# Kernel tuning notes

Measured on AMD Instinct MI355X. Metric: run time of the kernel, lower is better.

The kernel has to match this reference:

```python
import jax, jax.numpy as jnp
from jax import lax
import numpy as np

S, N, E = 4, 50000, 800000
D_IN, D_NOISE, D_H, D_OUT = 96, 32, 32, 128
F_CAT = D_IN + D_NOISE + D_H  # 160, matches nn.Linear(input_dim+noise_dim+32, out)


def setup_inputs() -> dict:
    key = jax.random.key(0)
    ks = jax.random.split(key, 8)
    X = jax.random.normal(ks[0], (1, N, D_IN), dtype=jnp.float32)
    h = jax.random.normal(ks[1], (1, N, D_H), dtype=jnp.float32)
    # Bernoulli(0.5) noise, sampled in setup for determinism (original samples in forward)
    epsilon = (jax.random.uniform(ks[2], (S, N, D_NOISE)) < 0.5).astype(jnp.float32)
    W = jax.random.normal(ks[3], (F_CAT, D_OUT), dtype=jnp.float32) * 0.02
    b = jnp.zeros((D_OUT,), dtype=jnp.float32)
    gin_eps = jnp.zeros((), dtype=jnp.float32)  # init_eps=0, learn_eps=True
    src = jax.random.randint(ks[4], (E,), 0, N, dtype=jnp.int32)
    dst = jax.random.randint(ks[5], (E,), 0, N, dtype=jnp.int32)
    return {"X": X, "h": h, "epsilon": epsilon, "W": W, "b": b,
            "gin_eps": gin_eps, "src": src, "dst": dst}


def reference(X, h, epsilon, W, b, gin_eps, src, dst):
    # X: [1,N,D_IN] expanded to sample_size; h: [1,N,32] expanded; epsilon: [S,N,D_NOISE]
    s, n = epsilon.shape[0], X.shape[1]
    Xb = jnp.broadcast_to(X, (s, n, X.shape[2]))
    hb = jnp.broadcast_to(h, (s, n, h.shape[2]))
    x_all = jnp.concatenate([Xb, epsilon, hb], axis=2)  # [S,N,F_CAT]

    def per_sample(carry, x):  # x: [N,F_CAT]
        # GINConv('sum'): (1+eps)*x + sum_{j in N(i)} x_j, then Linear, then activation
        agg = (1.0 + gin_eps) * x + jax.ops.segment_sum(x[src], dst, num_segments=n)
        y = jax.nn.relu(agg @ W + b)           # [N,D_OUT]
        return carry, jnp.mean(y, axis=0)      # per-layer mean over nodes -> [D_OUT]

    _, means = lax.scan(per_sample, None, x_all)  # [S,D_OUT]
    # outputTensor[i] = tempdim12 broadcasts the [D_OUT] vector over the node axis
    out = jnp.broadcast_to(means[:, None, :], (s, n, W.shape[1]))
    return jax.nn.relu(out), epsilon
```

## Files before the change

kernel.cpp:

```cpp
#include <hip/hip_runtime.h>

#define N_NODES  50000
#define N_EDGES  800000
#define D_OUTF   128
#define F_PACK   256
#define NTILES   3125
#define GEMM_BLOCKS 512
#define NB1      196
#define PBX 6250
#define PBB 25000
#define PBZ 196
#define PB_TOT (PBX + PBB + PBZ + 1)

typedef __attribute__((ext_vector_type(8))) short bf16x8;
typedef __attribute__((ext_vector_type(4))) float f32x4;
typedef __attribute__((ext_vector_type(2))) float f32x2;

__device__ __forceinline__ unsigned short f2bf(float x) {
  unsigned int u = __float_as_uint(x);
  u += 0x7FFFu + ((u >> 16) & 1u);
  return (unsigned short)(u >> 16);
}
__device__ __forceinline__ float bflo(unsigned int u) { return __uint_as_float(u << 16); }
__device__ __forceinline__ float bfhi(unsigned int u) { return __uint_as_float(u & 0xFFFF0000u); }
__device__ __forceinline__ unsigned int pack2(float a, float b) {
  return (unsigned int)f2bf(a) | ((unsigned int)f2bf(b) << 16);
}
__device__ __forceinline__ unsigned int spreadLo(unsigned int rep) {
  return (((rep & 0x08040201u) + 0x7F7F7F7Fu) >> 7) & 0x01010101u;
}
__device__ __forceinline__ unsigned int spreadHi(unsigned int rep) {
  return (((rep & 0x80402010u) + 0x7F7F7F7Fu) >> 7) & 0x01010101u;
}
__device__ __forceinline__ void f8acc(unsigned int w, float& a0, float& a1,
                                      float& a2, float& a3) {
  f32x2 p0 = __builtin_amdgcn_cvt_pk_f32_fp8(w, false);
  f32x2 p1 = __builtin_amdgcn_cvt_pk_f32_fp8(w, true);
  a0 += p0.x; a1 += p0.y; a2 += p1.x; a3 += p1.y;
}

__global__ void k_pack(const float* __restrict__ X, const float* __restrict__ h,
                       const float* __restrict__ eps,
                       unsigned int* __restrict__ featF8,
                       unsigned int* __restrict__ epsb, int* __restrict__ cnt,
                       float* __restrict__ sums) {
  int blk = blockIdx.x, tid = threadIdx.x;
  if (blk < PBX) {
    int t = blk * 256 + tid;
    int node = t >> 5, f = (t & 31) << 2;
    float a0, a1, a2, a3;
    if (f < 96) {
      const float* p = X + node * 96 + f;
      a0 = p[0]; a1 = p[1]; a2 = p[2]; a3 = p[3];
    } else {
      const float* p = h + node * 32 + (f - 96);
      a0 = p[0]; a1 = p[1]; a2 = p[2]; a3 = p[3];
    }
    unsigned int d = __builtin_amdgcn_cvt_pk_fp8_f32(a0, a1, 0, false);
    d = __builtin_amdgcn_cvt_pk_fp8_f32(a2, a3, d, true);
    featF8[t] = d;
  } else if (blk < PBX + PBB) {
    long g = (long)(blk - PBX) * 256 + tid;
    float v = eps[g];
    unsigned long long m = __ballot(v > 0.5f);
    int lane = tid & 63;
    if ((lane & 31) == 0) {
      long idx = g >> 5;
      int s = (int)(idx / N_NODES);
      int node = (int)(idx - (long)s * N_NODES);
      epsb[node * 4 + s] = (unsigned int)(m >> ((lane >> 5) * 32));
    }
  } else if (blk < PBX + PBB + PBZ) {
    int i = (blk - PBX - PBB) * 256 + tid;
    if (i < N_NODES) cnt[i] = 0;
  } else {
    sums[tid] = 0.f;
    sums[tid + 256] = 0.f;
  }
}

__global__ void k_hist(const int* __restrict__ dst, int* __restrict__ cnt) {
  int i = blockIdx.x * blockDim.x + threadIdx.x;
  if (i < N_EDGES) atomicAdd(&cnt[dst[i]], 1);
}

__global__ void k_scan1(const int* __restrict__ cnt, int* __restrict__ excl,
                        int* __restrict__ bsum) {
  __shared__ int wpart[4];
  int tid = threadIdx.x, lane = tid & 63, wid = tid >> 6;
  int i = blockIdx.x * 256 + tid;
  int v = (i < N_NODES) ? cnt[i] : 0;
  int x = v;
#pragma unroll
  for (int d = 1; d < 64; d <<= 1) {
    int t = __shfl_up(x, d, 64);
    if (lane >= d) x += t;
  }
  if (lane == 63) wpart[wid] = x;
  __syncthreads();
  if (tid == 0) {
    int s = 0;
#pragma unroll
    for (int w = 0; w < 4; ++w) { int t = wpart[w]; wpart[w] = s; s += t; }
    bsum[blockIdx.x] = s;
  }
  __syncthreads();
  if (i < N_NODES) excl[i] = wpart[wid] + x - v;
}

__global__ void k_scan2(const int* __restrict__ bsum, int* __restrict__ boff) {
  __shared__ int sd[256];
  int tid = threadIdx.x;
  int v = (tid < NB1) ? bsum[tid] : 0;
  sd[tid] = v;
  __syncthreads();
  for (int d = 1; d < 256; d <<= 1) {
    int t = (tid >= d) ? sd[tid - d] : 0;
    __syncthreads();
    sd[tid] += t;
    __syncthreads();
  }
  if (tid < NB1) boff[tid] = sd[tid] - v;
}

__global__ void k_scatter(const int* __restrict__ src, const int* __restrict__ dst,
                          const int* __restrict__ excl, const int* __restrict__ boff,
                          int* __restrict__ cnt, int* __restrict__ csr) {
  int i = blockIdx.x * blockDim.x + threadIdx.x;
  if (i < N_EDGES) {
    int d = dst[i];
    int r = atomicAdd(&cnt[d], -1);
    csr[excl[d] + boff[d >> 8] + r - 1] = src[i];
  }
}

__global__ __launch_bounds__(256) void k_agg_ep(
    const uint2* __restrict__ feat2, const unsigned int* __restrict__ epsw,
    const float* __restrict__ geps_p, const int* __restrict__ excl,
    const int* __restrict__ boff, const int* __restrict__ csr,
    uint4* __restrict__ agg4) {
  int wave = (blockIdx.x * blockDim.x + threadIdx.x) >> 6;
  int lane = threadIdx.x & 63;
  int li = lane & 15, es = lane >> 4;
  if (wave >= N_NODES) return;
  int n = wave;
  float ge = 1.0f + geps_p[0];
  int wsel = li >> 2, bsh = (li & 3) * 8;

  int off_n = excl[n] + boff[n >> 8];
  int e1 = (n == N_NODES - 1) ? N_EDGES : excl[n + 1] + boff[(n + 1) >> 8];

  uint2 sf = feat2[n * 16 + li];
  unsigned int swd = epsw[n * 4 + wsel];

  float af0 = 0.f, af1 = 0.f, af2 = 0.f, af3 = 0.f;
  float af4 = 0.f, af5 = 0.f, af6 = 0.f, af7 = 0.f;
  unsigned int accLo = 0, accHi = 0;

  int e = off_n + es;
  for (; e + 4 < e1; e += 8) {
    int s0 = csr[e], s1 = csr[e + 4];
    uint2 f0 = feat2[s0 * 16 + li];
    uint2 f1 = feat2[s1 * 16 + li];
    unsigned int w0 = epsw[s0 * 4 + wsel];
    unsigned int w1 = epsw[s1 * 4 + wsel];
    f8acc(f0.x, af0, af1, af2, af3);  f8acc(f0.y, af4, af5, af6, af7);
    f8acc(f1.x, af0, af1, af2, af3);  f8acc(f1.y, af4, af5, af6, af7);
    unsigned int B0 = (w0 >> bsh) & 0xFFu;
    unsigned int B1 = (w1 >> bsh) & 0xFFu;
    unsigned int r0 = B0 | (B0 << 8);  r0 |= r0 << 16;
    unsigned int r1 = B1 | (B1 << 8);  r1 |= r1 << 16;
    accLo += spreadLo(r0) + spreadLo(r1);
    accHi += spreadHi(r0) + spreadHi(r1);
  }
  if (e < e1) {
    int s0 = csr[e];
    uint2 f0 = feat2[s0 * 16 + li];
    unsigned int w0 = epsw[s0 * 4 + wsel];
    f8acc(f0.x, af0, af1, af2, af3);  f8acc(f0.y, af4, af5, af6, af7);
    unsigned int B0 = (w0 >> bsh) & 0xFFu;
    unsigned int r0 = B0 | (B0 << 8);  r0 |= r0 << 16;
    accLo += spreadLo(r0);
    accHi += spreadHi(r0);
  }

#pragma unroll
  for (int d = 16; d < 64; d <<= 1) {
    af0 += __shfl_xor(af0, d, 64);  af1 += __shfl_xor(af1, d, 64);
    af2 += __shfl_xor(af2, d, 64);  af3 += __shfl_xor(af3, d, 64);
    af4 += __shfl_xor(af4, d, 64);  af5 += __shfl_xor(af5, d, 64);
    af6 += __shfl_xor(af6, d, 64);  af7 += __shfl_xor(af7, d, 64);
    accLo += __shfl_xor((int)accLo, d, 64);
    accHi += __shfl_xor((int)accHi, d, 64);
  }

  if (es == 0) {
    f32x2 s0 = __builtin_amdgcn_cvt_pk_f32_fp8(sf.x, false);
    f32x2 s1 = __builtin_amdgcn_cvt_pk_f32_fp8(sf.x, true);
    f32x2 s2 = __builtin_amdgcn_cvt_pk_f32_fp8(sf.y, false);
    f32x2 s3 = __builtin_amdgcn_cvt_pk_f32_fp8(sf.y, true);
    af0 += ge * s0.x;  af1 += ge * s0.y;
    af2 += ge * s1.x;  af3 += ge * s1.y;
    af4 += ge * s2.x;  af5 += ge * s2.y;
    af6 += ge * s3.x;  af7 += ge * s3.y;
    unsigned int Bself = (swd >> bsh) & 0xFFu;
    float ev0 = ge * (float)(Bself & 1u)        + (float)(accLo & 0xFFu);
    float ev1 = ge * (float)((Bself >> 1) & 1u) + (float)((accLo >> 8) & 0xFFu);
    float ev2 = ge * (float)((Bself >> 2) & 1u) + (float)((accLo >> 16) & 0xFFu);
    float ev3 = ge * (float)((Bself >> 3) & 1u) + (float)((accLo >> 24) & 0xFFu);
    float ev4 = ge * (float)((Bself >> 4) & 1u) + (float)(accHi & 0xFFu);
    float ev5 = ge * (float)((Bself >> 5) & 1u) + (float)((accHi >> 8) & 0xFFu);
    float ev6 = ge * (float)((Bself >> 6) & 1u) + (float)((accHi >> 16) & 0xFFu);
    float ev7 = ge * (float)((Bself >> 7) & 1u) + (float)((accHi >> 24) & 0xFFu);

    uint4 oXh, oEp;
    oXh.x = pack2(af0, af1); oXh.y = pack2(af2, af3);
    oXh.z = pack2(af4, af5); oXh.w = pack2(af6, af7);
    oEp.x = pack2(ev0, ev1); oEp.y = pack2(ev2, ev3);
    oEp.z = pack2(ev4, ev5); oEp.w = pack2(ev6, ev7);
    agg4[n * 32 + li]      = oXh;
    agg4[n * 32 + 16 + li] = oEp;
  }
}

__global__ __launch_bounds__(256) void k_gemm(const unsigned short* __restrict__ agg,
    const float* __restrict__ W, const float* __restrict__ b,
    float* __restrict__ sums) {
  int tid = threadIdx.x;
  int lane = tid & 63;
  int w = tid >> 6;
  int col = lane & 15;
  int quad = lane >> 4;

  bf16x8 Bsh[2][4];
  bf16x8 Bep[2];
  float bias[2];
#pragma unroll
  for (int i = 0; i < 2; ++i) {
    int obase = (2 * w + i) * 16;
    bias[i] = b[obase + col];
#pragma unroll
    for (int kb = 0; kb < 4; ++kb) {
      bf16x8 f;
#pragma unroll
      for (int j = 0; j < 8; ++j) {
        int k = kb * 32 + quad * 8 + j;
        int wr = (k < 96) ? k : k + 32;
        f[j] = (short)f2bf(W[wr * D_OUTF + obase + col]);
      }
      Bsh[i][kb] = f;
    }
    bf16x8 g;
#pragma unroll
    for (int j = 0; j < 8; ++j)
      g[j] = (short)f2bf(W[(96 + quad * 8 + j) * D_OUTF + obase + col]);
    Bep[i] = g;
  }

  f32x4 psum[4][2];
#pragma unroll
  for (int s = 0; s < 4; ++s)
#pragma unroll
    for (int i = 0; i < 2; ++i) psum[s][i] = (f32x4){0.f, 0.f, 0.f, 0.f};

  for (int t = blockIdx.x; t < NTILES; t += gridDim.x) {
    const unsigned short* arow = agg + (long)(t * 16 + col) * F_PACK;
    bf16x8 Ash[4];
#pragma unroll
    for (int kb = 0; kb < 4; ++kb)
      Ash[kb] = *(const bf16x8*)(arow + kb * 32 + quad * 8);
    f32x4 csh[2];
    csh[0] = (f32x4){0.f, 0.f, 0.f, 0.f};
    csh[1] = (f32x4){0.f, 0.f, 0.f, 0.f};
#pragma unroll
    for (int kb = 0; kb < 4; ++kb) {
      csh[0] = __builtin_amdgcn_mfma_f32_16x16x32_bf16(Ash[kb], Bsh[0][kb], csh[0], 0, 0, 0);
      csh[1] = __builtin_amdgcn_mfma_f32_16x16x32_bf16(Ash[kb], Bsh[1][kb], csh[1], 0, 0, 0);
    }
#pragma unroll
    for (int s = 0; s < 4; ++s) {
      bf16x8 Aep = *(const bf16x8*)(arow + 128 + s * 32 + quad * 8);
#pragma unroll
      for (int i = 0; i < 2; ++i) {
        f32x4 c = __builtin_amdgcn_mfma_f32_16x16x32_bf16(Aep, Bep[i], csh[i], 0, 0, 0);
#pragma unroll
        for (int r = 0; r < 4; ++r)
          psum[s][i][r] += fmaxf(c[r] + bias[i], 0.f);
      }
    }
  }

#pragma unroll
  for (int s = 0; s < 4; ++s)
#pragma unroll
    for (int i = 0; i < 2; ++i) {
      float v = psum[s][i][0] + psum[s][i][1] + psum[s][i][2] + psum[s][i][3];
      v += __shfl_xor(v, 16, 64);
      v += __shfl_xor(v, 32, 64);
      if (quad == 0)
        atomicAdd(&sums[s * 128 + (2 * w + i) * 16 + col], v);
    }
}

#define OUT0_F4 6400000L
#define EPS_F4  1600000L
#define INV_N   (1.0f / (float)N_NODES)
__global__ void k_out(const float* __restrict__ sums, const float* __restrict__ eps,
                      float* __restrict__ out) {
  long i = (long)blockIdx.x * blockDim.x + threadIdx.x;
  if (i < OUT0_F4) {
    int o4 = (int)(i & 31);
    long sn = i >> 5;
    int s = (int)(sn / N_NODES);
    float4 sv = ((const float4*)sums)[s * 32 + o4];
    float4 ov;
    ov.x = fmaxf(sv.x * INV_N, 0.f);
    ov.y = fmaxf(sv.y * INV_N, 0.f);
    ov.z = fmaxf(sv.z * INV_N, 0.f);
    ov.w = fmaxf(sv.w * INV_N, 0.f);
    ((float4*)out)[i] = ov;
  } else if (i < OUT0_F4 + EPS_F4) {
    long j = i - OUT0_F4;
    ((float4*)out)[OUT0_F4 + j] = ((const float4*)eps)[j];
  }
}

extern "C" void kernel_launch(void* const* d_in, const int* in_sizes, int n_in,
                              void* d_out, int out_size, void* d_ws, size_t ws_size,
                              hipStream_t stream) {
  const float* X    = (const float*)d_in[0];
  const float* h    = (const float*)d_in[1];
  const float* eps  = (const float*)d_in[2];
  const float* W    = (const float*)d_in[3];
  const float* b    = (const float*)d_in[4];
  const float* geps = (const float*)d_in[5];
  const int*   src  = (const int*)d_in[6];
  const int*   dst  = (const int*)d_in[7];
  float* out = (float*)d_out;

  char* w = (char*)d_ws;
  unsigned int*  featF8 = (unsigned int*)w;  w += (size_t)N_NODES * 32 * 4;
  unsigned int*  epsb   = (unsigned int*)w;  w += (size_t)N_NODES * 4 * 4;
  unsigned int*  agg_u  = (unsigned int*)w;  w += (size_t)N_NODES * 128 * 4;
  int*   excl     = (int*)w;   w += (size_t)(N_NODES + 16) * 4;
  int*   cnt      = (int*)w;   w += (size_t)N_NODES * 4;
  int*   csr      = (int*)w;   w += (size_t)N_EDGES * 4;
  int*   bsum     = (int*)w;   w += 256 * 4;
  int*   boff     = (int*)w;   w += 256 * 4;
  float* sums     = (float*)w; w += 512 * 4;

  int eb = (N_EDGES + 255) / 256;
  k_pack<<<PB_TOT, 256, 0, stream>>>(X, h, eps, featF8, epsb, cnt, sums);
  k_hist<<<eb, 256, 0, stream>>>(dst, cnt);
  k_scan1<<<NB1, 256, 0, stream>>>(cnt, excl, bsum);
  k_scan2<<<1, 256, 0, stream>>>(bsum, boff);
  k_scatter<<<eb, 256, 0, stream>>>(src, dst, excl, boff, cnt, csr);

  k_agg_ep<<<(N_NODES * 64) / 256, 256, 0, stream>>>((const uint2*)featF8, epsb,
                                                     geps, excl, boff, csr,
                                                     (uint4*)agg_u);

  k_gemm<<<GEMM_BLOCKS, 256, 0, stream>>>((const unsigned short*)agg_u, W, b, sums);

  long total_f4 = OUT0_F4 + EPS_F4;
  k_out<<<(int)((total_f4 + 255) / 256), 256, 0, stream>>>(sums, eps, out);
}
```

Before: 333.6 us.

## Fuse scan passes, prepack W, copy epsilon in pack, deterministic last-block GEMM reduction

The second scan kernel is folded into the first through a last-block-done counter, which removes one launch. W is converted to bf16 and packed into MFMA fragment order once inside the pack kernel, so each GEMM block no longer does strided fp32 loads and conversions. The epsilon copy to the output is moved into the pack kernel, which already reads eps, so eps is not read a second time. GEMM blocks now write partial sums that the last block reduces, replacing float atomics, at the cost of a serial reduction over 512 partials in one block.

```diff
diff --git a/kernel.cpp b/kernel.cpp
--- a/kernel.cpp
+++ b/kernel.cpp
@@ -10,7 +10,12 @@
 #define PBX 6250
 #define PBB 25000
 #define PBZ 196
-#define PB_TOT (PBX + PBB + PBZ + 1)
+#define PBW 80
+#define PB_TOT (PBX + PBB + PBZ + PBW + 1)
+
+#define OUTB_F4  6400000
+#define EPS_OFF  25600000L
+#define INV_N    (1.0f / (float)N_NODES)
 
 typedef __attribute__((ext_vector_type(8))) short bf16x8;
 typedef __attribute__((ext_vector_type(4))) float f32x4;
@@ -21,8 +26,6 @@
   u += 0x7FFFu + ((u >> 16) & 1u);
   return (unsigned short)(u >> 16);
 }
-__device__ __forceinline__ float bflo(unsigned int u) { return __uint_as_float(u << 16); }
-__device__ __forceinline__ float bfhi(unsigned int u) { return __uint_as_float(u & 0xFFFF0000u); }
 __device__ __forceinline__ unsigned int pack2(float a, float b) {
   return (unsigned int)f2bf(a) | ((unsigned int)f2bf(b) << 16);
 }
@@ -40,10 +43,11 @@
 }
 
 __global__ void k_pack(const float* __restrict__ X, const float* __restrict__ h,
-                       const float* __restrict__ eps,
+                       const float* __restrict__ eps, const float* __restrict__ W,
                        unsigned int* __restrict__ featF8,
                        unsigned int* __restrict__ epsb, int* __restrict__ cnt,
-                       float* __restrict__ sums) {
+                       unsigned short* __restrict__ Wp,
+                       float* __restrict__ outEps, int* __restrict__ done) {
   int blk = blockIdx.x, tid = threadIdx.x;
   if (blk < PBX) {
     int t = blk * 256 + tid;
@@ -62,6 +66,7 @@
   } else if (blk < PBX + PBB) {
     long g = (long)(blk - PBX) * 256 + tid;
     float v = eps[g];
+    outEps[g] = v;
     unsigned long long m = __ballot(v > 0.5f);
     int lane = tid & 63;
     if ((lane & 31) == 0) {
@@ -73,9 +78,20 @@
   } else if (blk < PBX + PBB + PBZ) {
     int i = (blk - PBX - PBB) * 256 + tid;
     if (i < N_NODES) cnt[i] = 0;
+  } else if (blk < PBX + PBB + PBZ + PBW) {
+    int t = (blk - (PBX + PBB + PBZ)) * 256 + tid;
+    int j = t & 7, col = (t >> 3) & 15, quad = (t >> 7) & 3, r = t >> 9;
+    int kb5 = r % 5, i2 = r / 5;
+    int wr;
+    if (kb5 < 4) {
+      int k = kb5 * 32 + quad * 8 + j;
+      wr = (k < 96) ? k : k + 32;
+    } else {
+      wr = 96 + quad * 8 + j;
+    }
+    Wp[t] = f2bf(W[wr * D_OUTF + i2 * 16 + col]);
   } else {
-    sums[tid] = 0.f;
-    sums[tid + 256] = 0.f;
+    if (tid < 2) done[tid] = 0;
   }
 }
 
@@ -85,8 +101,11 @@
 }
 
 __global__ void k_scan1(const int* __restrict__ cnt, int* __restrict__ excl,
-                        int* __restrict__ bsum) {
+                        int* __restrict__ bsum, int* __restrict__ boff,
+                        int* __restrict__ done) {
   __shared__ int wpart[4];
+  __shared__ int sd[256];
+  __shared__ int lastf;
   int tid = threadIdx.x, lane = tid & 63, wid = tid >> 6;
   int i = blockIdx.x * 256 + tid;
   int v = (i < N_NODES) ? cnt[i] : 0;
@@ -102,25 +121,29 @@
     int s = 0;
 #pragma unroll
     for (int w = 0; w < 4; ++w) { int t = wpart[w]; wpart[w] = s; s += t; }
-    bsum[blockIdx.x] = s;
+    __hip_atomic_store(&bsum[blockIdx.x], s, __ATOMIC_RELEASE,
+                       __HIP_MEMORY_SCOPE_AGENT);
+    int d = __hip_atomic_fetch_add(done, 1, __ATOMIC_ACQ_REL,
+                                   __HIP_MEMORY_SCOPE_AGENT);
+    lastf = (d == NB1 - 1);
   }
   __syncthreads();
   if (i < N_NODES) excl[i] = wpart[wid] + x - v;
-}
-
-__global__ void k_scan2(const int* __restrict__ bsum, int* __restrict__ boff) {
-  __shared__ int sd[256];
-  int tid = threadIdx.x;
-  int v = (tid < NB1) ? bsum[tid] : 0;
-  sd[tid] = v;
-  __syncthreads();
-  for (int d = 1; d < 256; d <<= 1) {
-    int t = (tid >= d) ? sd[tid - d] : 0;
+  if (lastf) {
+    int bv = (tid < NB1)
+                 ? __hip_atomic_load(&bsum[tid], __ATOMIC_ACQUIRE,
+                                     __HIP_MEMORY_SCOPE_AGENT)
+                 : 0;
+    sd[tid] = bv;
     __syncthreads();
-    sd[tid] += t;
-    __syncthreads();
-  }
-  if (tid < NB1) boff[tid] = sd[tid] - v;
+    for (int d = 1; d < 256; d <<= 1) {
+      int t = (tid >= d) ? sd[tid - d] : 0;
+      __syncthreads();
+      sd[tid] += t;
+      __syncthreads();
+    }
+    if (tid < NB1) boff[tid] = sd[tid] - bv;
+  }
 }
 
 __global__ void k_scatter(const int* __restrict__ src, const int* __restrict__ dst,
@@ -224,37 +247,28 @@
 }
 
 __global__ __launch_bounds__(256) void k_gemm(const unsigned short* __restrict__ agg,
-    const float* __restrict__ W, const float* __restrict__ b,
-    float* __restrict__ sums) {
+    const unsigned short* __restrict__ Wp, const float* __restrict__ b,
+    float* __restrict__ partial, float* __restrict__ sums,
+    int* __restrict__ done2) {
+  __shared__ int lastf;
   int tid = threadIdx.x;
   int lane = tid & 63;
   int w = tid >> 6;
   int col = lane & 15;
   int quad = lane >> 4;
 
+  const bf16x8* wp8 = (const bf16x8*)Wp;
   bf16x8 Bsh[2][4];
   bf16x8 Bep[2];
   float bias[2];
 #pragma unroll
   for (int i = 0; i < 2; ++i) {
-    int obase = (2 * w + i) * 16;
-    bias[i] = b[obase + col];
-#pragma unroll
-    for (int kb = 0; kb < 4; ++kb) {
-      bf16x8 f;
-#pragma unroll
-      for (int j = 0; j < 8; ++j) {
-        int k = kb * 32 + quad * 8 + j;
-        int wr = (k < 96) ? k : k + 32;
-        f[j] = (short)f2bf(W[wr * D_OUTF + obase + col]);
-      }
-      Bsh[i][kb] = f;
-    }
-    bf16x8 g;
-#pragma unroll
-    for (int j = 0; j < 8; ++j)
-      g[j] = (short)f2bf(W[(96 + quad * 8 + j) * D_OUTF + obase + col]);
-    Bep[i] = g;
+    int i2 = 2 * w + i;
+    bias[i] = b[i2 * 16 + col];
+#pragma unroll
+    for (int kb = 0; kb < 4; ++kb)
+      Bsh[i][kb] = wp8[((i2 * 5 + kb) * 4 + quad) * 16 + col];
+    Bep[i] = wp8[((i2 * 5 + 4) * 4 + quad) * 16 + col];
   }
 
   f32x4 psum[4][2];
@@ -298,31 +312,41 @@
       v += __shfl_xor(v, 16, 64);
       v += __shfl_xor(v, 32, 64);
       if (quad == 0)
-        atomicAdd(&sums[s * 128 + (2 * w + i) * 16 + col], v);
-    }
-}
-
-#define OUT0_F4 6400000L
-#define EPS_F4  1600000L
-#define INV_N   (1.0f / (float)N_NODES)
-__global__ void k_out(const float* __restrict__ sums, const float* __restrict__ eps,
-                      float* __restrict__ out) {
-  long i = (long)blockIdx.x * blockDim.x + threadIdx.x;
-  if (i < OUT0_F4) {
-    int o4 = (int)(i & 31);
-    long sn = i >> 5;
-    int s = (int)(sn / N_NODES);
-    float4 sv = ((const float4*)sums)[s * 32 + o4];
-    float4 ov;
-    ov.x = fmaxf(sv.x * INV_N, 0.f);
-    ov.y = fmaxf(sv.y * INV_N, 0.f);
-    ov.z = fmaxf(sv.z * INV_N, 0.f);
-    ov.w = fmaxf(sv.w * INV_N, 0.f);
-    ((float4*)out)[i] = ov;
-  } else if (i < OUT0_F4 + EPS_F4) {
-    long j = i - OUT0_F4;
-    ((float4*)out)[OUT0_F4 + j] = ((const float4*)eps)[j];
-  }
+        partial[blockIdx.x * 512 + s * 128 + (2 * w + i) * 16 + col] = v;
+    }
+
+  __threadfence();
+  __syncthreads();
+  if (tid == 0) {
+    int d = __hip_atomic_fetch_add(done2, 1, __ATOMIC_ACQ_REL,
+                                   __HIP_MEMORY_SCOPE_AGENT);
+    lastf = (d == GEMM_BLOCKS - 1);
+  }
+  __syncthreads();
+  if (lastf) {
+    float a0 = 0.f, a1 = 0.f;
+#pragma unroll 4
+    for (int bb = 0; bb < GEMM_BLOCKS; ++bb) {
+      a0 += partial[(bb << 9) + tid];
+      a1 += partial[(bb << 9) + tid + 256];
+    }
+    sums[tid] = a0;
+    sums[tid + 256] = a1;
+  }
+}
+
+__global__ void k_out(const float* __restrict__ sums, float* __restrict__ out) {
+  int i = blockIdx.x * 256 + threadIdx.x;
+  int o4 = i & 31;
+  unsigned int sn = (unsigned int)i >> 5;
+  unsigned int s = sn / (unsigned int)N_NODES;
+  float4 sv = ((const float4*)sums)[s * 32 + o4];
+  float4 ov;
+  ov.x = fmaxf(sv.x * INV_N, 0.f);
+  ov.y = fmaxf(sv.y * INV_N, 0.f);
+  ov.z = fmaxf(sv.z * INV_N, 0.f);
+  ov.w = fmaxf(sv.w * INV_N, 0.f);
+  ((float4*)out)[i] = ov;
 }
 
 extern "C" void kernel_launch(void* const* d_in, const int* in_sizes, int n_in,
@@ -347,21 +371,24 @@
   int*   csr      = (int*)w;   w += (size_t)N_EDGES * 4;
   int*   bsum     = (int*)w;   w += 256 * 4;
   int*   boff     = (int*)w;   w += 256 * 4;
+  float* partial  = (float*)w; w += (size_t)GEMM_BLOCKS * 512 * 4;
+  unsigned short* Wp = (unsigned short*)w; w += (size_t)20480 * 2;
   float* sums     = (float*)w; w += 512 * 4;
+  int*   done     = (int*)w;   w += 64;
 
   int eb = (N_EDGES + 255) / 256;
-  k_pack<<<PB_TOT, 256, 0, stream>>>(X, h, eps, featF8, epsb, cnt, sums);
+  k_pack<<<PB_TOT, 256, 0, stream>>>(X, h, eps, W, featF8, epsb, cnt, Wp,
+                                     out + EPS_OFF, done);
   k_hist<<<eb, 256, 0, stream>>>(dst, cnt);
-  k_scan1<<<NB1, 256, 0, stream>>>(cnt, excl, bsum);
-  k_scan2<<<1, 256, 0, stream>>>(bsum, boff);
+  k_scan1<<<NB1, 256, 0, stream>>>(cnt, excl, bsum, boff, &done[0]);
   k_scatter<<<eb, 256, 0, stream>>>(src, dst, excl, boff, cnt, csr);
 
   k_agg_ep<<<(N_NODES * 64) / 256, 256, 0, stream>>>((const uint2*)featF8, epsb,
                                                      geps, excl, boff, csr,
                                                      (uint4*)agg_u);
 
-  k_gemm<<<GEMM_BLOCKS, 256, 0, stream>>>((const unsigned short*)agg_u, W, b, sums);
-
-  long total_f4 = OUT0_F4 + EPS_F4;
-  k_out<<<(int)((total_f4 + 255) / 256), 256, 0, stream>>>(sums, eps, out);
-}
+  k_gemm<<<GEMM_BLOCKS, 256, 0, stream>>>((const unsigned short*)agg_u, Wp, b,
+                                          partial, sums, &done[1]);
+
+  k_out<<<OUTB_F4 / 256, 256, 0, stream>>>(sums, out);
+}
```

Result: slower. 413.1 us (+23.8%).
